# Optimization experiments

Measured on AMD Instinct MI355X. Metric: run time of the kernel, lower is better.

## Reference

```python
import jax, jax.numpy as jnp
import numpy as np

N_EXPERTS, D_IN, D_OUT = 8, 1024, 1024
N_TOKENS = 8192


def setup_inputs() -> dict:
    key = jax.random.key(0)
    ks = jax.random.split(key, 5)
    s_in = 1.0 / np.sqrt(D_IN)
    x = jax.random.normal(ks[0], (N_TOKENS, D_IN), dtype=jnp.float32)
    W = jax.random.uniform(ks[1], (N_EXPERTS, D_IN, D_OUT), jnp.float32, -s_in, s_in)
    b = jax.random.uniform(ks[2], (N_EXPERTS, D_OUT), jnp.float32, -s_in, s_in)
    gate_W = jax.random.uniform(ks[3], (D_IN, N_EXPERTS), jnp.float32, -s_in, s_in)
    gate_b = jax.random.uniform(ks[4], (N_EXPERTS,), jnp.float32, -s_in, s_in)
    return {"x": x, "W": W, "b": b, "gate_W": gate_W, "gate_b": gate_b}


def reference(x, W, b, gate_W, gate_b):
    # gate: [n, e] softmax over experts
    gate_score = jax.nn.softmax(x @ gate_W + gate_b, axis=-1)
    # all experts applied densely: [n, e, o]
    expert_outputs = jnp.einsum('ni,eio->neo', x, W) + b[None, :, :]
    # weighted combine over expert axis: [n, o]
    return jnp.einsum('ne,neo->no', gate_score, expert_outputs)
```

## Files before the change

### kernel.cpp

```cpp
#include <hip/hip_runtime.h>
#include <hip/hip_bf16.h>
#include <cstdint>
#include <cstddef>

#define N_TOK 8192
#define D_IN  1024
#define D_OUT 1024
#define N_EXP 8
#define KTOT  (N_EXP * D_IN)

#define BM    256
#define BN    128
#define BKH   32
#define NSTEP 256

typedef __attribute__((ext_vector_type(8))) short short8;
typedef __attribute__((ext_vector_type(8))) unsigned short ushort8;
typedef __attribute__((ext_vector_type(4))) float f32x4;

__device__ __forceinline__ unsigned short f2bf(float f) {
    union { float f; unsigned int u; } v; v.f = f;
    return (unsigned short)((v.u + 0x7FFFu + ((v.u >> 16) & 1u)) >> 16);
}

__device__ __forceinline__ void load_lds16(const void* g, void* l) {
    __builtin_amdgcn_global_load_lds(
        (const __attribute__((address_space(1))) void*)g,
        (__attribute__((address_space(3))) void*)l,
        16, 0, 0);
}

__global__ __launch_bounds__(256) void prep_kernel(
    const float* __restrict__ x, const float* __restrict__ gW,
    const float* __restrict__ gbias, const float* __restrict__ W,
    unsigned short* __restrict__ xb, unsigned short* __restrict__ Wt,
    float* __restrict__ g_t) {
    const int b = blockIdx.x;
    const int t = threadIdx.x;

    if (b < 2048) {
        __shared__ float tile[64][65];
        const int e  = b >> 8;
        const int i0 = ((b >> 4) & 15) * 64;
        const int o0 = (b & 15) * 64;

        const int rr = t >> 4;
        const int rc = (t & 15) * 4;
#pragma unroll
        for (int j = 0; j < 4; ++j) {
            const float4 v = *(const float4*)(
                W + ((size_t)e * D_IN + (i0 + rr + 16 * j)) * D_OUT + o0 + rc);
            tile[rr + 16 * j][rc + 0] = v.x;
            tile[rr + 16 * j][rc + 1] = v.y;
            tile[rr + 16 * j][rc + 2] = v.z;
            tile[rr + 16 * j][rc + 3] = v.w;
        }
        __syncthreads();
        const int ow = t >> 2;
        const int c  = (t & 3) * 16;
        ushort8 v0, v1;
#pragma unroll
        for (int j = 0; j < 8; ++j) v0[j] = f2bf(tile[c + j][ow]);
#pragma unroll
        for (int j = 0; j < 8; ++j) v1[j] = f2bf(tile[c + 8 + j][ow]);
        unsigned short* dst = Wt + (size_t)(o0 + ow) * KTOT + e * D_IN + i0 + c;
        *(ushort8*)dst = v0;
        *(ushort8*)(dst + 8) = v1;
    } else {
        const int lane = t & 63;
        const int n    = (b - 2048) * 4 + (t >> 6);

        float acc[8];
#pragma unroll
        for (int e = 0; e < 8; ++e) acc[e] = 0.f;
#pragma unroll
        for (int jj = 0; jj < 4; ++jj) {
            const int i = 256 * jj + 4 * lane;
            const float4 xv = *(const float4*)(x + (size_t)n * D_IN + i);
            ushort4 u;
            u.x = f2bf(xv.x); u.y = f2bf(xv.y);
            u.z = f2bf(xv.z); u.w = f2bf(xv.w);
            *(ushort4*)(xb + (size_t)n * D_IN + i) = u;
            const float xs[4] = {xv.x, xv.y, xv.z, xv.w};
#pragma unroll
            for (int j = 0; j < 4; ++j) {
                const float* wr = gW + (size_t)(i + j) * N_EXP;
                const float4 w0 = *(const float4*)wr;
                const float4 w1 = *(const float4*)(wr + 4);
                acc[0] += xs[j] * w0.x; acc[1] += xs[j] * w0.y;
                acc[2] += xs[j] * w0.z; acc[3] += xs[j] * w0.w;
                acc[4] += xs[j] * w1.x; acc[5] += xs[j] * w1.y;
                acc[6] += xs[j] * w1.z; acc[7] += xs[j] * w1.w;
            }
        }
#pragma unroll
        for (int off = 32; off > 0; off >>= 1) {
#pragma unroll
            for (int e = 0; e < 8; ++e) acc[e] += __shfl_down(acc[e], off);
        }
        if (lane == 0) {
            float lg[8], mx = -1e30f;
#pragma unroll
            for (int e = 0; e < 8; ++e) {
                lg[e] = acc[e] + gbias[e];
                mx = fmaxf(mx, lg[e]);
            }
            float s = 0.f;
#pragma unroll
            for (int e = 0; e < 8; ++e) { lg[e] = expf(lg[e] - mx); s += lg[e]; }
            const float inv = 1.f / s;
#pragma unroll
            for (int e = 0; e < 8; ++e)
                g_t[(size_t)e * N_TOK + n] = lg[e] * inv;
        }
    }
}

__global__ __launch_bounds__(512, 1) void moe_gemm13_kernel(
    const unsigned short* __restrict__ xb,
    const unsigned short* __restrict__ Wt,
    const float* __restrict__ bias,
    const float* __restrict__ g_t,
    float* __restrict__ out) {
    __shared__ __align__(16) unsigned short A4[4][BM * BKH];
    __shared__ __align__(16) unsigned short B4[4][BN * BKH];
    __shared__ __align__(16) float g_s[N_EXP][BM];
    __shared__ __align__(16) float r_s[N_EXP][BM];
    __shared__ __align__(16) float b_s[N_EXP][BN];

    const int t    = threadIdx.x;
    const int lane = t & 63;
    const int ln15 = lane & 15;
    const int quad = lane >> 4;
    const int wave = t >> 6;
    const int wm0  = (wave >> 1) * 64;
    const int wn0  = (wave & 1) * 64;

    const int flat = blockIdx.x + 8 * blockIdx.y;
    const int bn0  = ((flat >> 3) & 7) * BN;
    const int bm0  = ((flat & 7) * 4 + (flat >> 6)) * BM;

    for (int j = t; j < N_EXP * BM; j += 512)
        g_s[j >> 8][j & 255] = g_t[(size_t)(j >> 8) * N_TOK + bm0 + (j & 255)];
    for (int j = t; j < N_EXP * BN; j += 512)
        b_s[j >> 7][j & 127] = bias[(size_t)(j >> 7) * D_OUT + bn0 + (j & 127)];
    __syncthreads();
    if (t < BM) {
        float d[N_EXP];
#pragma unroll
        for (int e = 0; e < N_EXP; ++e) d[e] = fmaxf(g_s[e][t], 1e-30f);
#pragma unroll
        for (int e = 1; e < N_EXP; ++e) r_s[e][t] = d[e - 1] / d[e];
        r_s[0][t] = d[N_EXP - 1];
    }
    __syncthreads();

    f32x4 acc[4][4];
#pragma unroll
    for (int mi = 0; mi < 4; ++mi)
#pragma unroll
        for (int ni = 0; ni < 4; ++ni)
            acc[mi][ni] = (f32x4){0.f, 0.f, 0.f, 0.f};

    const int srow = t >> 2;
    const int csw  = ((t & 3) ^ ((t >> 3) & 3)) * 8;
    const unsigned short* gA = xb + (size_t)(bm0 + srow) * D_IN + csw;
    const unsigned short* gB = Wt + (size_t)(bn0 + srow) * (size_t)KTOT + csw;
    const int wrow = wave * 16 * BKH;

    const int ksw  = (quad ^ ((ln15 >> 1) & 3)) * 8;
    const int aoff = (wm0 + ln15) * BKH + ksw;
    const int boff = (wn0 + ln15) * BKH + ksw;

    short8 afA[4], bvA[4], afB[4], bvB[4];

#pragma unroll
    for (int s = 0; s < 3; ++s) {
        load_lds16(gA + s * BKH,              &A4[s][wrow]);
        load_lds16(gA + 128 * D_IN + s * BKH, &A4[s][128 * BKH + wrow]);
        load_lds16(gB + (size_t)s * BKH,      &B4[s][wrow]);
    }
    asm volatile("s_waitcnt vmcnt(3)" ::: "memory");
    __builtin_amdgcn_s_barrier();
    __builtin_amdgcn_sched_barrier(0);
#pragma unroll
    for (int mi = 0; mi < 4; ++mi)
        afA[mi] = *(const short8*)(&A4[0][0] + aoff + mi * 16 * BKH);
#pragma unroll
    for (int ni = 0; ni < 4; ++ni)
        bvA[ni] = *(const short8*)(&B4[0][0] + boff + ni * 16 * BKH);

#define MFMA4(CUR, mi_)                                                       \
    _Pragma("unroll") for (int ni = 0; ni < 4; ++ni)                          \
        acc[mi_][ni] = __builtin_amdgcn_mfma_f32_16x16x32_bf16(               \
            af##CUR[mi_], bv##CUR[ni], acc[mi_][ni], 0, 0, 0);

#define STEP(h_, CUR, NXT, DO_STAGE, DO_READ)                                 \
  {                                                                           \
    const int hs_ = (h_) + 3;                                                 \
    const unsigned short* An_ = &A4[((h_) + 1) & 3][0];                       \
    const unsigned short* Bn_ = &B4[((h_) + 1) & 3][0];                       \
    asm volatile("s_waitcnt lgkmcnt(0)" ::: "memory");                        \
    __builtin_amdgcn_sched_barrier(0);                                        \
    if ((h_) && !((h_) & 31)) {      \
      const int e_ = (h_) >> 5;                                               \
      _Pragma("unroll") for (int mi = 0; mi < 4; ++mi) {                      \
        const f32x4 rv = *(const f32x4*)&r_s[e_][wm0 + mi * 16 + quad * 4];   \
        _Pragma("unroll") for (int ni = 0; ni < 4; ++ni)                      \
          _Pragma("unroll") for (int r = 0; r < 4; ++r)                       \
            acc[mi][ni][r] *= rv[r];                                          \
      }                                                                       \
    }                                                                         \
    __builtin_amdgcn_s_setprio(1);                                            \
    MFMA4(CUR, 0)                                                             \
    __builtin_amdgcn_sched_barrier(0);                                        \
    if (DO_READ) {                                                            \
      af##NXT[0] = *(const short8*)(An_ + aoff + 0 * 16 * BKH);               \
      af##NXT[1] = *(const short8*)(An_ + aoff + 1 * 16 * BKH);               \
    }                                                                         \
    __builtin_amdgcn_sched_barrier(0);                                        \
    MFMA4(CUR, 1)                                                             \
    __builtin_amdgcn_sched_barrier(0);                                        \
    if (DO_READ) {                                                            \
      af##NXT[2] = *(const short8*)(An_ + aoff + 2 * 16 * BKH);               \
      af##NXT[3] = *(const short8*)(An_ + aoff + 3 * 16 * BKH);               \
    }                                                                         \
    __builtin_amdgcn_sched_barrier(0);                                        \
    MFMA4(CUR, 2)                                                             \
    __builtin_amdgcn_sched_barrier(0);                                        \
    if (DO_READ) {                                                            \
      _Pragma("unroll") for (int ni = 0; ni < 4; ++ni)                        \
        bv##NXT[ni] = *(const short8*)(Bn_ + boff + ni * 16 * BKH);           \
    }                                                                         \
    __builtin_amdgcn_sched_barrier(0);                                        \
    MFMA4(CUR, 3)                                                             \
    __builtin_amdgcn_s_setprio(0);                                            \
    __builtin_amdgcn_sched_barrier(0);                                        \
    if (DO_STAGE) {                                                           \
      load_lds16(gA + ((hs_) & 31) * BKH,              &A4[(hs_) & 3][wrow]); \
      load_lds16(gA + 128 * D_IN + ((hs_) & 31) * BKH,                        \
                 &A4[(hs_) & 3][128 * BKH + wrow]);                           \
      load_lds16(gB + (size_t)(hs_) * BKH,             &B4[(hs_) & 3][wrow]); \
    }                                                                         \
  }

#define ENDW(N_)                                                              \
  asm volatile("s_waitcnt vmcnt(" #N_ ")" ::: "memory");                      \
  __builtin_amdgcn_s_barrier();                                               \
  __builtin_amdgcn_sched_barrier(0);

    for (int h = 0; h < NSTEP - 4; h += 2) {
        STEP(h, A, B, 1, 1);
        ENDW(3);
        STEP(h + 1, B, A, 1, 1);
        ENDW(3);
    }
    STEP(252, A, B, 1, 1);
    ENDW(3);
    STEP(253, B, A, 0, 1);
    ENDW(0);
    STEP(254, A, B, 0, 1);
    STEP(255, B, A, 0, 0);

#undef STEP
#undef MFMA4
#undef ENDW

#pragma unroll
    for (int mi = 0; mi < 4; ++mi) {
        const f32x4 fin = *(const f32x4*)&r_s[0][wm0 + mi * 16 + quad * 4];
#pragma unroll
        for (int ni = 0; ni < 4; ++ni)
#pragma unroll
            for (int r = 0; r < 4; ++r) acc[mi][ni][r] *= fin[r];
    }
#pragma unroll
    for (int e = 0; e < N_EXP; ++e) {
        f32x4 gv[4];
        float bb[4];
#pragma unroll
        for (int mi = 0; mi < 4; ++mi)
            gv[mi] = *(const f32x4*)&g_s[e][wm0 + mi * 16 + quad * 4];
#pragma unroll
        for (int ni = 0; ni < 4; ++ni) bb[ni] = b_s[e][wn0 + ni * 16 + ln15];
#pragma unroll
        for (int mi = 0; mi < 4; ++mi)
#pragma unroll
            for (int ni = 0; ni < 4; ++ni)
#pragma unroll
                for (int r = 0; r < 4; ++r)
                    acc[mi][ni][r] += gv[mi][r] * bb[ni];
    }

#pragma unroll
    for (int mi = 0; mi < 4; ++mi) {
#pragma unroll
        for (int ni = 0; ni < 4; ++ni) {
            const int col  = bn0 + wn0 + ni * 16 + ln15;
            const int row0 = bm0 + wm0 + mi * 16 + quad * 4;
#pragma unroll
            for (int r = 0; r < 4; ++r)
                out[(size_t)(row0 + r) * D_OUT + col] = acc[mi][ni][r];
        }
    }
}

extern "C" void kernel_launch(void* const* d_in, const int* in_sizes, int n_in,
                              void* d_out, int out_size, void* d_ws, size_t ws_size,
                              hipStream_t stream) {
    const float* x  = (const float*)d_in[0];
    const float* W  = (const float*)d_in[1];
    const float* b  = (const float*)d_in[2];
    const float* gW = (const float*)d_in[3];
    const float* gb = (const float*)d_in[4];
    float* out = (float*)d_out;

    unsigned short* xb  = (unsigned short*)d_ws;
    unsigned short* Wt  = xb + (size_t)N_TOK * D_IN;
    float*          g_t = (float*)(Wt + (size_t)D_OUT * KTOT);

    prep_kernel<<<4096, 256, 0, stream>>>(x, gW, gb, W, xb, Wt, g_t);
    moe_gemm13_kernel<<<dim3(D_OUT / BN, N_TOK / BM), 512, 0, stream>>>(
        xb, Wt, b, g_t, out);
}
```

Baseline: 263.5 us.

## Load B fragments directly from global into registers, bypassing LDS staging

The weight operand B no longer goes through a 4-stage LDS ring. Each wave now loads its own B MFMA fragments straight from global memory into registers, one step ahead. The A-tile staging and the B prefetch are moved to the start of each step, and the wait counts are adjusted to match. This removes LDS writes, LDS reads and LDS footprint for B. In exchange, waves that share a B column slice load it redundantly from L2. Global-load latency also has to be hidden within a single step, because the barrier wait now forces the B loads to complete.

Result: slower. 469.2 us (+78.1%).

```diff
diff --git a/kernel.cpp b/kernel.cpp
--- a/kernel.cpp
+++ b/kernel.cpp
@@ -116,14 +116,13 @@
     }
 }
 
-__global__ __launch_bounds__(512, 1) void moe_gemm13_kernel(
+__global__ __launch_bounds__(512, 1) void moe_gemm14_kernel(
     const unsigned short* __restrict__ xb,
     const unsigned short* __restrict__ Wt,
     const float* __restrict__ bias,
     const float* __restrict__ g_t,
     float* __restrict__ out) {
     __shared__ __align__(16) unsigned short A4[4][BM * BKH];
-    __shared__ __align__(16) unsigned short B4[4][BN * BKH];
     __shared__ __align__(16) float g_s[N_EXP][BM];
     __shared__ __align__(16) float r_s[N_EXP][BM];
     __shared__ __align__(16) float b_s[N_EXP][BN];
@@ -162,44 +161,52 @@
         for (int ni = 0; ni < 4; ++ni)
             acc[mi][ni] = (f32x4){0.f, 0.f, 0.f, 0.f};
 
-    const int srow = t >> 2;
     const int csw  = ((t & 3) ^ ((t >> 3) & 3)) * 8;
-    const unsigned short* gA = xb + (size_t)(bm0 + srow) * D_IN + csw;
-    const unsigned short* gB = Wt + (size_t)(bn0 + srow) * (size_t)KTOT + csw;
+    const unsigned short* gA = xb + (size_t)(bm0 + (t >> 2)) * D_IN + csw;
     const int wrow = wave * 16 * BKH;
 
     const int ksw  = (quad ^ ((ln15 >> 1) & 3)) * 8;
     const int aoff = (wm0 + ln15) * BKH + ksw;
-    const int boff = (wn0 + ln15) * BKH + ksw;
-
-    short8 afA[4], bvA[4], afB[4], bvB[4];
-
+
+    const unsigned short* gBf =
+        Wt + (size_t)(bn0 + wn0 + ln15) * KTOT + quad * 8;
+
+    short8 afA[4], afB[4], bvA[4], bvB[4];
+
+#pragma unroll
+    for (int ni = 0; ni < 4; ++ni)
+        bvA[ni] = *(const short8*)(gBf + (size_t)ni * 16 * KTOT);
 #pragma unroll
     for (int s = 0; s < 3; ++s) {
         load_lds16(gA + s * BKH,              &A4[s][wrow]);
         load_lds16(gA + 128 * D_IN + s * BKH, &A4[s][128 * BKH + wrow]);
-        load_lds16(gB + (size_t)s * BKH,      &B4[s][wrow]);
-    }
-    asm volatile("s_waitcnt vmcnt(3)" ::: "memory");
+    }
+    asm volatile("s_waitcnt vmcnt(2)" ::: "memory");
     __builtin_amdgcn_s_barrier();
     __builtin_amdgcn_sched_barrier(0);
 #pragma unroll
     for (int mi = 0; mi < 4; ++mi)
         afA[mi] = *(const short8*)(&A4[0][0] + aoff + mi * 16 * BKH);
-#pragma unroll
-    for (int ni = 0; ni < 4; ++ni)
-        bvA[ni] = *(const short8*)(&B4[0][0] + boff + ni * 16 * BKH);
 
 #define MFMA4(CUR, mi_)                                                       \
     _Pragma("unroll") for (int ni = 0; ni < 4; ++ni)                          \
         acc[mi_][ni] = __builtin_amdgcn_mfma_f32_16x16x32_bf16(               \
             af##CUR[mi_], bv##CUR[ni], acc[mi_][ni], 0, 0, 0);
 
-#define STEP(h_, CUR, NXT, DO_STAGE, DO_READ)                                 \
+#define STEP(h_, CUR, NXT, DO_STAGE, DO_BLOAD, DO_READ)                       \
   {                                                                           \
     const int hs_ = (h_) + 3;                                                 \
     const unsigned short* An_ = &A4[((h_) + 1) & 3][0];                       \
-    const unsigned short* Bn_ = &B4[((h_) + 1) & 3][0];                       \
+    if (DO_BLOAD) {                                                           \
+      _Pragma("unroll") for (int ni = 0; ni < 4; ++ni)                        \
+        bv##NXT[ni] = *(const short8*)(                                       \
+            gBf + (size_t)ni * 16 * KTOT + ((h_) + 1) * 32);                  \
+    }                                                                         \
+    if (DO_STAGE) {                                                           \
+      load_lds16(gA + ((hs_) & 31) * BKH,              &A4[(hs_) & 3][wrow]); \
+      load_lds16(gA + 128 * D_IN + ((hs_) & 31) * BKH,                        \
+                 &A4[(hs_) & 3][128 * BKH + wrow]);                           \
+    }                                                                         \
     asm volatile("s_waitcnt lgkmcnt(0)" ::: "memory");                        \
     __builtin_amdgcn_sched_barrier(0);                                        \
     if ((h_) && !((h_) & 31)) {      \
@@ -214,34 +221,24 @@
     __builtin_amdgcn_s_setprio(1);                                            \
     MFMA4(CUR, 0)                                                             \
     __builtin_amdgcn_sched_barrier(0);                                        \
-    if (DO_READ) {                                                            \
+    if (DO_READ)                                                              \
       af##NXT[0] = *(const short8*)(An_ + aoff + 0 * 16 * BKH);               \
+    __builtin_amdgcn_sched_barrier(0);                                        \
+    MFMA4(CUR, 1)                                                             \
+    __builtin_amdgcn_sched_barrier(0);                                        \
+    if (DO_READ)                                                              \
       af##NXT[1] = *(const short8*)(An_ + aoff + 1 * 16 * BKH);               \
-    }                                                                         \
-    __builtin_amdgcn_sched_barrier(0);                                        \
-    MFMA4(CUR, 1)                                                             \
+    __builtin_amdgcn_sched_barrier(0);                                        \
+    MFMA4(CUR, 2)                                                             \
     __builtin_amdgcn_sched_barrier(0);                                        \
     if (DO_READ) {                                                            \
       af##NXT[2] = *(const short8*)(An_ + aoff + 2 * 16 * BKH);               \
       af##NXT[3] = *(const short8*)(An_ + aoff + 3 * 16 * BKH);               \
     }                                                                         \
     __builtin_amdgcn_sched_barrier(0);                                        \
-    MFMA4(CUR, 2)                                                             \
-    __builtin_amdgcn_sched_barrier(0);                                        \
-    if (DO_READ) {                                                            \
-      _Pragma("unroll") for (int ni = 0; ni < 4; ++ni)                        \
-        bv##NXT[ni] = *(const short8*)(Bn_ + boff + ni * 16 * BKH);           \
-    }                                                                         \
-    __builtin_amdgcn_sched_barrier(0);                                        \
     MFMA4(CUR, 3)                                                             \
     __builtin_amdgcn_s_setprio(0);                                            \
     __builtin_amdgcn_sched_barrier(0);                                        \
-    if (DO_STAGE) {                                                           \
-      load_lds16(gA + ((hs_) & 31) * BKH,              &A4[(hs_) & 3][wrow]); \
-      load_lds16(gA + 128 * D_IN + ((hs_) & 31) * BKH,                        \
-                 &A4[(hs_) & 3][128 * BKH + wrow]);                           \
-      load_lds16(gB + (size_t)(hs_) * BKH,             &B4[(hs_) & 3][wrow]); \
-    }                                                                         \
   }
 
 #define ENDW(N_)                                                              \
@@ -250,17 +247,18 @@
   __builtin_amdgcn_sched_barrier(0);
 
     for (int h = 0; h < NSTEP - 4; h += 2) {
-        STEP(h, A, B, 1, 1);
-        ENDW(3);
-        STEP(h + 1, B, A, 1, 1);
-        ENDW(3);
-    }
-    STEP(252, A, B, 1, 1);
-    ENDW(3);
-    STEP(253, B, A, 0, 1);
+        STEP(h, A, B, 1, 1, 1);
+        ENDW(2);
+        STEP(h + 1, B, A, 1, 1, 1);
+        ENDW(2);
+    }
+    STEP(252, A, B, 1, 1, 1);
+    ENDW(2);
+    STEP(253, B, A, 0, 1, 1);
     ENDW(0);
-    STEP(254, A, B, 0, 1);
-    STEP(255, B, A, 0, 0);
+    STEP(254, A, B, 0, 1, 1);
+    ENDW(0);
+    STEP(255, B, A, 0, 0, 0);
 
 #undef STEP
 #undef MFMA4
@@ -320,6 +318,6 @@
     float*          g_t = (float*)(Wt + (size_t)D_OUT * KTOT);
 
     prep_kernel<<<4096, 256, 0, stream>>>(x, gW, gb, W, xb, Wt, g_t);
-    moe_gemm13_kernel<<<dim3(D_OUT / BN, N_TOK / BM), 512, 0, stream>>>(
+    moe_gemm14_kernel<<<dim3(D_OUT / BN, N_TOK / BM), 512, 0, stream>>>(
         xb, Wt, b, g_t, out);
 }
```
